# Performance work log

Measured on AMD Instinct MI355X. Metric: run time of the kernel, lower is better.

The kernel has to match this reference:

```python
import jax, jax.numpy as jnp
import numpy as np

B, D, C = 1024, 128, 100000
EPS = 1e-12  # torch F.normalize eps


def setup_inputs() -> dict:
    key = jax.random.key(0)
    k1, k2, k3 = jax.random.split(key, 3)
    # scale so ||x||^2 ~ 1, keeping exp(-dist) in a representable range
    xs = jax.random.normal(k1, (B, D), dtype=jnp.float32) / np.sqrt(D)
    ys = jax.random.randint(k2, (B,), 0, C, dtype=jnp.int64)
    # xavier_uniform init of Embedding(C, D): U(-a, a), a = sqrt(6/(C+D))
    a = np.sqrt(6.0 / (C + D))
    proxies = jax.random.uniform(k3, (C, D), dtype=jnp.float32, minval=-a, maxval=a)
    return {"xs": xs, "ys": ys, "proxies": proxies}


def reference(xs, ys, proxies):
    # L2-normalize every proxy (original normalizes pos proxy over dim=0 of a 1-D
    # vector and neg proxies over dim=1 -- both are per-proxy L2 normalization).
    norm = jnp.linalg.norm(proxies, axis=1, keepdims=True)
    P = proxies / jnp.maximum(norm, EPS)                      # [C, D], unit rows
    x_sq = jnp.sum(xs * xs, axis=1, keepdims=True)            # [B, 1]
    d = x_sq + 1.0 - 2.0 * (xs @ P.T)                         # [B, C]
    e = jnp.exp(-d)                                           # [B, C]
    pos = jnp.take_along_axis(e, ys[:, None], axis=1)[:, 0]   # exp(-d[b, y_b])
    neg_sum = jnp.sum(e, axis=1) - pos                        # denominator excludes the positive
    return jnp.mean(-jnp.log(pos / neg_sum))
```

## Files before the change

kernel.cpp:

```cpp
#include <hip/hip_runtime.h>
#include <hip/hip_fp16.h>

#define B_N 1024
#define D_K 128
#define C_N 100000
#define CT_PER_CHUNK 5
#define CCHUNK (CT_PER_CHUNK * 32)
#define NCHUNK (C_N / CCHUNK)
#define BSPLIT 2
#define NBLK_MAIN (NCHUNK * BSPLIT)
#define NREP 64
#define K2LOG2E 2.8853900817779268f
#define EPSN 1e-12f

typedef _Float16 half8 __attribute__((ext_vector_type(8)));
typedef float floatx16 __attribute__((ext_vector_type(16)));

union U16 { uint4 u; half8 h; };

#define EXP2F(x) __builtin_amdgcn_exp2f(x)

__device__ __forceinline__ unsigned int pack2h(float a, float b) {
    union { _Float16 h[2]; unsigned int u; } p;
    p.h[0] = (_Float16)a; p.h[1] = (_Float16)b;
    return p.u;
}

__global__ __launch_bounds__(256) void prep_kernel(
    const float* __restrict__ xs, const int* __restrict__ ys,
    const float* __restrict__ proxies,
    unsigned int* __restrict__ xfrag, float* __restrict__ w,
    float* __restrict__ posd, float* __restrict__ negsumR)
{
    int tid = threadIdx.x, bb = blockIdx.x;
    negsumR[bb * 256 + tid] = 0.0f;

    int wave = tid >> 6, lane = tid & 63;
    int b = bb * 4 + wave;
    const float2 xv = ((const float2*)(xs + (size_t)b * D_K))[lane];
    float ss = xv.x * xv.x + xv.y * xv.y;
    #pragma unroll
    for (int m = 1; m < 64; m <<= 1) ss += __shfl_xor(ss, m, 64);
    float xsq = ss;

    int ks = lane >> 3, kh = (lane >> 2) & 1, jq = lane & 3;
    int idx = (((b >> 5) * 8 + ks) * 64 + ((b & 31) | (kh << 5))) * 4 + jq;
    xfrag[idx] = pack2h(K2LOG2E * xv.x, K2LOG2E * xv.y);

    int y = ys[b];
    const float2 pv = ((const float2*)(proxies + (size_t)y * D_K))[lane];
    float dt = xv.x * pv.x + xv.y * pv.y;
    float pp = pv.x * pv.x + pv.y * pv.y;
    #pragma unroll
    for (int m = 1; m < 64; m <<= 1) {
        dt += __shfl_xor(dt, m, 64);
        pp += __shfl_xor(pp, m, 64);
    }
    if (lane == 0) {
        w[b] = __expf(-xsq - 1.0f);
        float nrm = fmaxf(sqrtf(pp), EPSN);
        posd[b] = xsq + 1.0f - 2.0f * (dt / nrm);
    }
}

__device__ __forceinline__ void compute_pair(
    const uint4* ldsP, int lane,
    const uint4 xfA[8], const uint4 xfB[8],
    float& outA, float& outB)
{
    float sA0 = 0.f, sA1 = 0.f, sB0 = 0.f, sB1 = 0.f;
    #pragma unroll 1
    for (int ct = 0; ct < CT_PER_CHUNK; ++ct) {
        uint4 a[8];
        #pragma unroll
        for (int k = 0; k < 8; ++k)
            a[k] = ldsP[(ct * 8 + k) * 64 + lane];

        floatx16 accA, accB;
        #pragma unroll
        for (int i = 0; i < 16; ++i) { accA[i] = 0.0f; accB[i] = 0.0f; }

        #pragma unroll
        for (int k = 0; k < 8; ++k) {
            U16 ua, u0, u1;
            ua.u = a[k]; u0.u = xfA[k]; u1.u = xfB[k];
            accA = __builtin_amdgcn_mfma_f32_32x32x16_f16(ua.h, u0.h, accA, 0, 0, 0);
            accB = __builtin_amdgcn_mfma_f32_32x32x16_f16(ua.h, u1.h, accB, 0, 0, 0);
        }

        #pragma unroll
        for (int i = 0; i < 16; i += 2) {
            sA0 += EXP2F(accA[i]);     sA1 += EXP2F(accA[i + 1]);
            sB0 += EXP2F(accB[i]);     sB1 += EXP2F(accB[i + 1]);
        }
    }
    outA = sA0 + sA1;
    outB = sB0 + sB1;
}

__global__ __launch_bounds__(256, 3) void main_kernel(
    const float* __restrict__ proxies,
    const uint4* __restrict__ xfrag,
    const float* __restrict__ w, float* __restrict__ negsumR)
{
    __shared__ uint4 ldsP[CT_PER_CHUNK * 8 * 64];

    int tid = threadIdx.x, wave = tid >> 6, lane = tid & 63;
    int bx = blockIdx.x;
    int c0 = (bx >> 1) * CCHUNK;
    int bs = bx & 1;

    {
        int L = tid & 7;
        int r = tid >> 3;
        #pragma unroll 1
        for (int p = 0; p < CT_PER_CHUNK; ++p) {
            int c = c0 + p * 32 + r;
            const float4* src = (const float4*)(proxies + (size_t)c * D_K + L * 16);
            float4 v0 = src[0], v1 = src[1], v2 = src[2], v3 = src[3];
            float ss = v0.x*v0.x + v0.y*v0.y + v0.z*v0.z + v0.w*v0.w
                     + v1.x*v1.x + v1.y*v1.y + v1.z*v1.z + v1.w*v1.w
                     + v2.x*v2.x + v2.y*v2.y + v2.z*v2.z + v2.w*v2.w
                     + v3.x*v3.x + v3.y*v3.y + v3.z*v3.z + v3.w*v3.w;
            ss += __shfl_xor(ss, 1, 64);
            ss += __shfl_xor(ss, 2, 64);
            ss += __shfl_xor(ss, 4, 64);
            float sc = 1.0f / fmaxf(sqrtf(ss), EPSN);

            union { _Float16 h[8]; uint4 u; } pa, pb;
            pa.h[0]=(_Float16)(v0.x*sc); pa.h[1]=(_Float16)(v0.y*sc);
            pa.h[2]=(_Float16)(v0.z*sc); pa.h[3]=(_Float16)(v0.w*sc);
            pa.h[4]=(_Float16)(v1.x*sc); pa.h[5]=(_Float16)(v1.y*sc);
            pa.h[6]=(_Float16)(v1.z*sc); pa.h[7]=(_Float16)(v1.w*sc);
            pb.h[0]=(_Float16)(v2.x*sc); pb.h[1]=(_Float16)(v2.y*sc);
            pb.h[2]=(_Float16)(v2.z*sc); pb.h[3]=(_Float16)(v2.w*sc);
            pb.h[4]=(_Float16)(v3.x*sc); pb.h[5]=(_Float16)(v3.y*sc);
            pb.h[6]=(_Float16)(v3.z*sc); pb.h[7]=(_Float16)(v3.w*sc);

            ldsP[p * 512 + L * 64 + r]      = pa.u;
            ldsP[p * 512 + L * 64 + 32 + r] = pb.u;
        }
    }

    int nt0 = bs * 16 + wave * 4;
    uint4 xfA[8], xfB[8];
    #pragma unroll
    for (int k = 0; k < 8; ++k) xfA[k] = xfrag[((nt0    ) * 8 + k) * 64 + lane];
    #pragma unroll
    for (int k = 0; k < 8; ++k) xfB[k] = xfrag[((nt0 + 1) * 8 + k) * 64 + lane];

    __syncthreads();

    int rep = bx & (NREP - 1);
    float* nsr = negsumR + (size_t)rep * B_N;

    float s0, s1;
    compute_pair(ldsP, lane, xfA, xfB, s0, s1);

    #pragma unroll
    for (int k = 0; k < 8; ++k) xfA[k] = xfrag[((nt0 + 2) * 8 + k) * 64 + lane];
    #pragma unroll
    for (int k = 0; k < 8; ++k) xfB[k] = xfrag[((nt0 + 3) * 8 + k) * 64 + lane];

    s0 += __shfl_xor(s0, 32, 64);
    s1 += __shfl_xor(s1, 32, 64);
    if (lane < 32) {
        int b0 = (nt0    ) * 32 + lane;
        int b1 = (nt0 + 1) * 32 + lane;
        atomicAdd(&nsr[b0], s0 * w[b0]);
        atomicAdd(&nsr[b1], s1 * w[b1]);
    }

    float s2, s3;
    compute_pair(ldsP, lane, xfA, xfB, s2, s3);
    s2 += __shfl_xor(s2, 32, 64);
    s3 += __shfl_xor(s3, 32, 64);
    if (lane < 32) {
        int b2 = (nt0 + 2) * 32 + lane;
        int b3 = (nt0 + 3) * 32 + lane;
        atomicAdd(&nsr[b2], s2 * w[b2]);
        atomicAdd(&nsr[b3], s3 * w[b3]);
    }
}

__global__ __launch_bounds__(1024) void final_kernel(
    const float* __restrict__ negsumR, const float* __restrict__ posd,
    float* __restrict__ out)
{
    __shared__ float red[1024];
    int t = threadIdx.x;
    float ns = 0.0f;
    #pragma unroll 4
    for (int r = 0; r < NREP; ++r) ns += negsumR[r * B_N + t];
    float pd = posd[t];
    red[t] = logf(ns - __expf(-pd)) + pd;
    __syncthreads();
    #pragma unroll
    for (int s = 512; s > 0; s >>= 1) {
        if (t < s) red[t] += red[t + s];
        __syncthreads();
    }
    if (t == 0) out[0] = red[0] * (1.0f / 1024.0f);
}

extern "C" void kernel_launch(void* const* d_in, const int* in_sizes, int n_in,
                              void* d_out, int out_size, void* d_ws, size_t ws_size,
                              hipStream_t stream)
{
    const float* xs      = (const float*)d_in[0];
    const int*   ys      = (const int*)d_in[1];
    const float* proxies = (const float*)d_in[2];

    char* ws = (char*)d_ws;
    unsigned int* xfrag   = (unsigned int*)ws;
    float*        w       = (float*)(ws + 262144);
    float*        posd    = (float*)(ws + 262144 + 4096);
    float*        negsumR = (float*)(ws + 262144 + 8192);

    prep_kernel<<<256, 256, 0, stream>>>(xs, ys, proxies, xfrag, w, posd, negsumR);
    main_kernel<<<NBLK_MAIN, 256, 0, stream>>>(proxies, (const uint4*)xfrag, w, negsumR);
    final_kernel<<<1, 1024, 0, stream>>>(negsumR, posd, (float*)d_out);
}
```

Before: 125.3 us.

## Make main kernel persistent with double-buffered proxy tiles and swizzled LDS

Replaces the one-chunk-per-block grid (1250 blocks loading 5 tiles up front) with 1024 persistent blocks that stride over 32-row proxy tiles. The next tile's global load overlaps the MFMA/exp work on the current tile through a two-buffer LDS ring. All four x fragments are kept in registers for the whole loop, and atomics are issued once per block at the end. LDS writes and reads use an XOR swizzle to avoid bank conflicts. In exchange there is higher register pressure (occupancy hint drops from 3 to 2 blocks) and a barrier per tile.

```diff
diff --git a/kernel.cpp b/kernel.cpp
--- a/kernel.cpp
+++ b/kernel.cpp
@@ -4,11 +4,9 @@
 #define B_N 1024
 #define D_K 128
 #define C_N 100000
-#define CT_PER_CHUNK 5
-#define CCHUNK (CT_PER_CHUNK * 32)
-#define NCHUNK (C_N / CCHUNK)
-#define BSPLIT 2
-#define NBLK_MAIN (NCHUNK * BSPLIT)
+#define NTILE 3125
+#define NPAIR 512
+#define NBLK_MAIN (NPAIR * 2)
 #define NREP 64
 #define K2LOG2E 2.8853900817779268f
 #define EPSN 1e-12f
@@ -63,123 +61,118 @@
     }
 }
 
-__device__ __forceinline__ void compute_pair(
-    const uint4* ldsP, int lane,
-    const uint4 xfA[8], const uint4 xfB[8],
-    float& outA, float& outB)
-{
-    float sA0 = 0.f, sA1 = 0.f, sB0 = 0.f, sB1 = 0.f;
+__device__ __forceinline__ void stage_write(
+    uint4* dst, int L, int r, float4 v0, float4 v1, float4 v2, float4 v3)
+{
+    float ss = v0.x*v0.x + v0.y*v0.y + v0.z*v0.z + v0.w*v0.w
+             + v1.x*v1.x + v1.y*v1.y + v1.z*v1.z + v1.w*v1.w
+             + v2.x*v2.x + v2.y*v2.y + v2.z*v2.z + v2.w*v2.w
+             + v3.x*v3.x + v3.y*v3.y + v3.z*v3.z + v3.w*v3.w;
+    ss += __shfl_xor(ss, 1, 64);
+    ss += __shfl_xor(ss, 2, 64);
+    ss += __shfl_xor(ss, 4, 64);
+    float sc = 1.0f / fmaxf(sqrtf(ss), EPSN);
+
+    union { _Float16 h[8]; uint4 u; } pa, pb;
+    pa.h[0]=(_Float16)(v0.x*sc); pa.h[1]=(_Float16)(v0.y*sc);
+    pa.h[2]=(_Float16)(v0.z*sc); pa.h[3]=(_Float16)(v0.w*sc);
+    pa.h[4]=(_Float16)(v1.x*sc); pa.h[5]=(_Float16)(v1.y*sc);
+    pa.h[6]=(_Float16)(v1.z*sc); pa.h[7]=(_Float16)(v1.w*sc);
+    pb.h[0]=(_Float16)(v2.x*sc); pb.h[1]=(_Float16)(v2.y*sc);
+    pb.h[2]=(_Float16)(v2.z*sc); pb.h[3]=(_Float16)(v2.w*sc);
+    pb.h[4]=(_Float16)(v3.x*sc); pb.h[5]=(_Float16)(v3.y*sc);
+    pb.h[6]=(_Float16)(v3.z*sc); pb.h[7]=(_Float16)(v3.w*sc);
+
+    int sl = r ^ L;
+    dst[L * 64 + sl]      = pa.u;
+    dst[L * 64 + 32 + sl] = pb.u;
+}
+
+__global__ __launch_bounds__(256, 2) void main_kernel(
+    const float* __restrict__ proxies,
+    const uint4* __restrict__ xfrag,
+    const float* __restrict__ w, float* __restrict__ negsumR)
+{
+    __shared__ uint4 ldsP[2][512];
+
+    int tid = threadIdx.x, wave = tid >> 6, lane = tid & 63;
+    int bx = blockIdx.x;
+    int pairId = bx >> 1;
+    int bs = bx & 1;
+    int L = tid & 7, r = tid >> 3;
+    int nt0 = bs * 16 + wave * 4;
+
+    int tile0 = pairId;
+    float4 p0, p1, p2, p3;
+    {
+        const float4* src = (const float4*)(proxies + (size_t)(tile0 * 32 + r) * D_K + L * 16);
+        p0 = src[0]; p1 = src[1]; p2 = src[2]; p3 = src[3];
+    }
+
+    uint4 xf[4][8];
+    #pragma unroll
+    for (int nt = 0; nt < 4; ++nt)
+        #pragma unroll
+        for (int k = 0; k < 8; ++k)
+            xf[nt][k] = xfrag[((nt0 + nt) * 8 + k) * 64 + lane];
+
+    stage_write(ldsP[0], L, r, p0, p1, p2, p3);
+    __syncthreads();
+
+    float s0 = 0.f, s1 = 0.f, s2 = 0.f, s3 = 0.f;
+    int buf = 0;
+
     #pragma unroll 1
-    for (int ct = 0; ct < CT_PER_CHUNK; ++ct) {
+    for (int tile = tile0; tile < NTILE; tile += NPAIR) {
+        int nxt = tile + NPAIR;
+        bool have = nxt < NTILE;
+        if (have) {
+            const float4* src = (const float4*)(proxies + (size_t)(nxt * 32 + r) * D_K + L * 16);
+            p0 = src[0]; p1 = src[1]; p2 = src[2]; p3 = src[3];
+        }
+
         uint4 a[8];
         #pragma unroll
         for (int k = 0; k < 8; ++k)
-            a[k] = ldsP[(ct * 8 + k) * 64 + lane];
-
-        floatx16 accA, accB;
+            a[k] = ldsP[buf][k * 64 + (lane ^ k)];
+
         #pragma unroll
-        for (int i = 0; i < 16; ++i) { accA[i] = 0.0f; accB[i] = 0.0f; }
-
-        #pragma unroll
-        for (int k = 0; k < 8; ++k) {
-            U16 ua, u0, u1;
-            ua.u = a[k]; u0.u = xfA[k]; u1.u = xfB[k];
-            accA = __builtin_amdgcn_mfma_f32_32x32x16_f16(ua.h, u0.h, accA, 0, 0, 0);
-            accB = __builtin_amdgcn_mfma_f32_32x32x16_f16(ua.h, u1.h, accB, 0, 0, 0);
+        for (int h = 0; h < 2; ++h) {
+            floatx16 accA, accB;
+            #pragma unroll
+            for (int i = 0; i < 16; ++i) { accA[i] = 0.0f; accB[i] = 0.0f; }
+            #pragma unroll
+            for (int k = 0; k < 8; ++k) {
+                U16 ua, u0, u1;
+                ua.u = a[k]; u0.u = xf[2*h][k]; u1.u = xf[2*h+1][k];
+                accA = __builtin_amdgcn_mfma_f32_32x32x16_f16(ua.h, u0.h, accA, 0, 0, 0);
+                accB = __builtin_amdgcn_mfma_f32_32x32x16_f16(ua.h, u1.h, accB, 0, 0, 0);
+            }
+            float tA0 = 0.f, tA1 = 0.f, tB0 = 0.f, tB1 = 0.f;
+            #pragma unroll
+            for (int i = 0; i < 16; i += 2) {
+                tA0 += EXP2F(accA[i]);   tA1 += EXP2F(accA[i + 1]);
+                tB0 += EXP2F(accB[i]);   tB1 += EXP2F(accB[i + 1]);
+            }
+            if (h == 0) { s0 += tA0 + tA1; s1 += tB0 + tB1; }
+            else        { s2 += tA0 + tA1; s3 += tB0 + tB1; }
         }
 
-        #pragma unroll
-        for (int i = 0; i < 16; i += 2) {
-            sA0 += EXP2F(accA[i]);     sA1 += EXP2F(accA[i + 1]);
-            sB0 += EXP2F(accB[i]);     sB1 += EXP2F(accB[i + 1]);
-        }
-    }
-    outA = sA0 + sA1;
-    outB = sB0 + sB1;
-}
-
-__global__ __launch_bounds__(256, 3) void main_kernel(
-    const float* __restrict__ proxies,
-    const uint4* __restrict__ xfrag,
-    const float* __restrict__ w, float* __restrict__ negsumR)
-{
-    __shared__ uint4 ldsP[CT_PER_CHUNK * 8 * 64];
-
-    int tid = threadIdx.x, wave = tid >> 6, lane = tid & 63;
-    int bx = blockIdx.x;
-    int c0 = (bx >> 1) * CCHUNK;
-    int bs = bx & 1;
-
-    {
-        int L = tid & 7;
-        int r = tid >> 3;
-        #pragma unroll 1
-        for (int p = 0; p < CT_PER_CHUNK; ++p) {
-            int c = c0 + p * 32 + r;
-            const float4* src = (const float4*)(proxies + (size_t)c * D_K + L * 16);
-            float4 v0 = src[0], v1 = src[1], v2 = src[2], v3 = src[3];
-            float ss = v0.x*v0.x + v0.y*v0.y + v0.z*v0.z + v0.w*v0.w
-                     + v1.x*v1.x + v1.y*v1.y + v1.z*v1.z + v1.w*v1.w
-                     + v2.x*v2.x + v2.y*v2.y + v2.z*v2.z + v2.w*v2.w
-                     + v3.x*v3.x + v3.y*v3.y + v3.z*v3.z + v3.w*v3.w;
-            ss += __shfl_xor(ss, 1, 64);
-            ss += __shfl_xor(ss, 2, 64);
-            ss += __shfl_xor(ss, 4, 64);
-            float sc = 1.0f / fmaxf(sqrtf(ss), EPSN);
-
-            union { _Float16 h[8]; uint4 u; } pa, pb;
-            pa.h[0]=(_Float16)(v0.x*sc); pa.h[1]=(_Float16)(v0.y*sc);
-            pa.h[2]=(_Float16)(v0.z*sc); pa.h[3]=(_Float16)(v0.w*sc);
-            pa.h[4]=(_Float16)(v1.x*sc); pa.h[5]=(_Float16)(v1.y*sc);
-            pa.h[6]=(_Float16)(v1.z*sc); pa.h[7]=(_Float16)(v1.w*sc);
-            pb.h[0]=(_Float16)(v2.x*sc); pb.h[1]=(_Float16)(v2.y*sc);
-            pb.h[2]=(_Float16)(v2.z*sc); pb.h[3]=(_Float16)(v2.w*sc);
-            pb.h[4]=(_Float16)(v3.x*sc); pb.h[5]=(_Float16)(v3.y*sc);
-            pb.h[6]=(_Float16)(v3.z*sc); pb.h[7]=(_Float16)(v3.w*sc);
-
-            ldsP[p * 512 + L * 64 + r]      = pa.u;
-            ldsP[p * 512 + L * 64 + 32 + r] = pb.u;
-        }
-    }
-
-    int nt0 = bs * 16 + wave * 4;
-    uint4 xfA[8], xfB[8];
-    #pragma unroll
-    for (int k = 0; k < 8; ++k) xfA[k] = xfrag[((nt0    ) * 8 + k) * 64 + lane];
-    #pragma unroll
-    for (int k = 0; k < 8; ++k) xfB[k] = xfrag[((nt0 + 1) * 8 + k) * 64 + lane];
-
-    __syncthreads();
+        if (have) stage_write(ldsP[buf ^ 1], L, r, p0, p1, p2, p3);
+        __syncthreads();
+        buf ^= 1;
+    }
 
     int rep = bx & (NREP - 1);
     float* nsr = negsumR + (size_t)rep * B_N;
-
-    float s0, s1;
-    compute_pair(ldsP, lane, xfA, xfB, s0, s1);
-
-    #pragma unroll
-    for (int k = 0; k < 8; ++k) xfA[k] = xfrag[((nt0 + 2) * 8 + k) * 64 + lane];
-    #pragma unroll
-    for (int k = 0; k < 8; ++k) xfB[k] = xfrag[((nt0 + 3) * 8 + k) * 64 + lane];
-
-    s0 += __shfl_xor(s0, 32, 64);
-    s1 += __shfl_xor(s1, 32, 64);
-    if (lane < 32) {
-        int b0 = (nt0    ) * 32 + lane;
-        int b1 = (nt0 + 1) * 32 + lane;
-        atomicAdd(&nsr[b0], s0 * w[b0]);
-        atomicAdd(&nsr[b1], s1 * w[b1]);
-    }
-
-    float s2, s3;
-    compute_pair(ldsP, lane, xfA, xfB, s2, s3);
-    s2 += __shfl_xor(s2, 32, 64);
-    s3 += __shfl_xor(s3, 32, 64);
-    if (lane < 32) {
-        int b2 = (nt0 + 2) * 32 + lane;
-        int b3 = (nt0 + 3) * 32 + lane;
-        atomicAdd(&nsr[b2], s2 * w[b2]);
-        atomicAdd(&nsr[b3], s3 * w[b3]);
+    float vs[4] = {s0, s1, s2, s3};
+    #pragma unroll
+    for (int nt = 0; nt < 4; ++nt) {
+        float v = vs[nt] + __shfl_xor(vs[nt], 32, 64);
+        if (lane < 32) {
+            int b = (nt0 + nt) * 32 + lane;
+            atomicAdd(&nsr[b], v * w[b]);
+        }
     }
 }
 
@@ -191,7 +184,7 @@
     int t = threadIdx.x;
     float ns = 0.0f;
     #pragma unroll 4
-    for (int r = 0; r < NREP; ++r) ns += negsumR[r * B_N + t];
+    for (int rr = 0; rr < NREP; ++rr) ns += negsumR[rr * B_N + t];
     float pd = posd[t];
     red[t] = logf(ns - __expf(-pd)) + pd;
     __syncthreads();
```

Measured after the change: 124.2 us. About the same (-0.8%).
